# Performance work log

Measured on AMD Instinct MI355X. Metric: run time of the kernel, lower is better.

## Reference

```python
import jax, jax.numpy as jnp
import numpy as np

D = 512      # model_dim
H = 8        # num_heads
HD = D // H  # head_dim = 64
S = 196      # tokens per channel (14x14 grid)
CHANNELS = np.array([2, 4, 6, 4], dtype=np.int32)  # multiplex channels per sample


def setup_inputs() -> dict:
    key = jax.random.key(0)
    ks = jax.random.split(key, 8)
    C = int(CHANNELS.sum())  # 16
    n = lambda k, shp, s=1.0: jax.random.normal(k, shp, dtype=jnp.float32) * s
    return {
        "x_query": n(ks[0], (C, S, D)),
        "x_keyval": n(ks[1], (C, S, D)),
        "pos": n(ks[2], (C, S, D)),
        "channels": CHANNELS,
        "Wq": n(ks[3], (D, D), 0.02), "bq": jnp.zeros((D,), jnp.float32),
        "Wk": n(ks[4], (D, D), 0.02), "bk": jnp.zeros((D,), jnp.float32),
        "Wv": n(ks[5], (D, D), 0.02), "bv": jnp.zeros((D,), jnp.float32),
        "Wo": n(ks[6], (D, D), 0.02), "bo": jnp.zeros((D,), jnp.float32),
    }


def reference(x_query, x_keyval, pos, channels, Wq, bq, Wk, bk, Wv, bv, Wo, bo):
    C, S_, D_ = x_query.shape
    ch = np.asarray(channels)
    # segment id per packed token; segment i has length channels[i]*S (== cu_seq_len blocks)
    seg = np.repeat(np.arange(ch.shape[0]), ch * S_)                # [T] static
    block_mask = seg[:, None] == seg[None, :]                        # [T,T] static bool

    xq = x_query.reshape(-1, D_)   # [T,D]
    xk = x_keyval.reshape(-1, D_)
    p = pos.reshape(-1, D_)

    # positional embedding fused into Q/K before projection (query_pos/key_pos)
    q = ((xq + p) @ Wq + bq).reshape(-1, H, HD)
    k = ((xk + p) @ Wk + bk).reshape(-1, H, HD)
    v = (xk @ Wv + bv).reshape(-1, H, HD)

    scale = 1.0 / np.sqrt(HD)
    scores = jnp.einsum('qhd,khd->hqk', q, k) * scale               # [H,T,T]
    scores = jnp.where(block_mask[None], scores, jnp.float32(-1e30))
    attn = jax.nn.softmax(scores, axis=-1)
    out = jnp.einsum('hqk,khd->qhd', attn, v).reshape(-1, D_)       # [T,D]
    out = out @ Wo + bo
    return out.reshape(C, S_, D_)
```

## Files before the change

### kernel.cpp

```cpp
#include <hip/hip_runtime.h>
#include <hip/hip_bf16.h>


typedef short short8 __attribute__((ext_vector_type(8)));
typedef float f32x4 __attribute__((ext_vector_type(4)));

__device__ __forceinline__ float b2f(unsigned short u) {
    union { float f; unsigned int i; } x; x.i = ((unsigned int)u) << 16; return x.f;
}
__device__ __forceinline__ unsigned short f2b(float f) {
    union { float f; unsigned int i; } x; x.f = f;
    unsigned int r = x.i + 0x7fffu + ((x.i >> 16) & 1u);
    return (unsigned short)(r >> 16);
}

#define NE 1605632
#define WE 262144
#define GS 72

__launch_bounds__(256)
__global__ void prep(const float* __restrict__ xq, const float* __restrict__ xk,
                     const float* __restrict__ pos,
                     const float* __restrict__ W0, const float* __restrict__ W1,
                     const float* __restrict__ W2, const float* __restrict__ W3,
                     unsigned short* __restrict__ WF,
                     unsigned short* __restrict__ aqb, unsigned short* __restrict__ akb,
                     unsigned short* __restrict__ xkbb) {
    const int tid = threadIdx.x;
    if (blockIdx.z < 4) {
        if (blockIdx.x >= 128) return;
        const float* W = blockIdx.z == 0 ? W0 : blockIdx.z == 1 ? W1 : blockIdx.z == 2 ? W2 : W3;
        unsigned short* T = WF + (size_t)blockIdx.z * WE;
        const int s = blockIdx.x * 4 + (tid >> 6);
        const int f = s >> 4, t = s & 15;
        const int lane = tid & 63, quad = lane >> 4, l16 = lane & 15;
        short8 o;
        #pragma unroll
        for (int j = 0; j < 8; ++j)
            o[j] = (short)f2b(W[(size_t)(t * 32 + quad * 8 + j) * 512 + f * 16 + l16]);
        *(short8*)(T + (size_t)s * 512 + lane * 8) = o;
    } else {
        const size_t e = ((size_t)blockIdx.x * 256 + tid) * 8;
        f32x4 q0 = *(const f32x4*)(xq + e),  q1 = *(const f32x4*)(xq + e + 4);
        f32x4 k0 = *(const f32x4*)(xk + e),  k1 = *(const f32x4*)(xk + e + 4);
        f32x4 p0 = *(const f32x4*)(pos + e), p1 = *(const f32x4*)(pos + e + 4);
        short8 a, b, c;
        #pragma unroll
        for (int j = 0; j < 4; ++j) {
            a[j] = (short)f2b(q0[j] + p0[j]); a[4 + j] = (short)f2b(q1[j] + p1[j]);
            b[j] = (short)f2b(k0[j] + p0[j]); b[4 + j] = (short)f2b(k1[j] + p1[j]);
            c[j] = (short)f2b(k0[j]);         c[4 + j] = (short)f2b(k1[j]);
        }
        *(short8*)(aqb + e)  = a;
        *(short8*)(akb + e)  = b;
        *(short8*)(xkbb + e) = c;
    }
}

template <bool OUT_F32>
__device__ __forceinline__ void gemm_wave(const unsigned short* __restrict__ A,
                                          const unsigned short* __restrict__ WFw,
                                          const float* __restrict__ bias,
                                          void* __restrict__ C,
                                          int m0, int n0) {
    const int lane = threadIdx.x & 63;
    const int quad = lane >> 4, l16 = lane & 15;
    const int f0 = n0 >> 4;
    const unsigned short* Arow = A + (size_t)(m0 + l16) * 512 + quad * 8;
    const unsigned short* Bbase = WFw + (size_t)lane * 8;

    f32x4 acc[4] = {};
    #pragma unroll 4
    for (int t = 0; t < 16; ++t) {
        short8 af = *(const short8*)(Arow + t * 32);
        #pragma unroll
        for (int nt = 0; nt < 4; ++nt) {
            short8 bf = *(const short8*)(Bbase + (size_t)((f0 + nt) * 16 + t) * 512);
            acc[nt] = __builtin_amdgcn_mfma_f32_16x16x32_bf16(af, bf, acc[nt], 0, 0, 0);
        }
    }
    #pragma unroll
    for (int nt = 0; nt < 4; ++nt) {
        const int col = n0 + nt * 16 + l16;
        const float bv = bias[col];
        #pragma unroll
        for (int r = 0; r < 4; ++r) {
            const int row = m0 + quad * 4 + r;
            float cv = acc[nt][r] + bv;
            if constexpr (OUT_F32) ((float*)C)[(size_t)row * 512 + col] = cv;
            else ((unsigned short*)C)[(size_t)row * 512 + col] = f2b(cv);
        }
    }
}

__launch_bounds__(256)
__global__ void qkv_gemm(const unsigned short* __restrict__ aqb,
                         const unsigned short* __restrict__ akb,
                         const unsigned short* __restrict__ xkbb,
                         const unsigned short* __restrict__ WF,
                         const float* __restrict__ bq, const float* __restrict__ bk,
                         const float* __restrict__ bv,
                         unsigned short* __restrict__ qb, unsigned short* __restrict__ kb,
                         unsigned short* __restrict__ vb) {
    const unsigned short* A; const unsigned short* WFw; const float* bias; unsigned short* C;
    switch (blockIdx.z) {
        case 0:  A = aqb;  WFw = WF;          bias = bq; C = qb; break;
        case 1:  A = akb;  WFw = WF + WE;     bias = bk; C = kb; break;
        default: A = xkbb; WFw = WF + 2 * WE; bias = bv; C = vb; break;
    }
    gemm_wave<false>(A, WFw, bias, C, blockIdx.x * 64 + (threadIdx.x >> 6) * 16,
                     blockIdx.y * 64);
}

__launch_bounds__(256)
__global__ void out_gemm(const unsigned short* __restrict__ A,
                         const unsigned short* __restrict__ WFo,
                         const float* __restrict__ bo, float* __restrict__ out) {
    gemm_wave<true>(A, WFo, bo, out, blockIdx.x * 64 + (threadIdx.x >> 6) * 16,
                    blockIdx.y * 64);
}

__launch_bounds__(256)
__global__ void attn_seg(const unsigned short* __restrict__ q,
                         const unsigned short* __restrict__ k,
                         const unsigned short* __restrict__ v,
                         unsigned short* __restrict__ o) {
    __shared__ __align__(16) unsigned short Vt[64 * GS];
    __shared__ __align__(16) unsigned char  Pw[4][16 * 144];

    const int id = blockIdx.x;
    int h, off, L, qt;
    if (id < 152)      { h = id & 7; qt = id >> 3; off = 1176; L = 1176; }
    else if (id < 360) { int m = id - 152; h = m & 7; int s = m >> 3;
                         if (s < 13) { off = 392;  L = 784; qt = s; }
                         else        { off = 2352; L = 784; qt = s - 13; } }
    else               { int m = id - 360; h = m & 7; qt = m >> 3; off = 0; L = 392; }

    const int tid = threadIdx.x;
    const int wave = tid >> 6, lane = tid & 63;
    const int quad = lane >> 4, l16 = lane & 15;
    const int hb = h * 64;
    const int lastr = off + L - 1;

    int qrow = off + qt * 64 + wave * 16 + l16;
    if (qrow > lastr) qrow = lastr;
    const short8 qf0 = *(const short8*)(q + (size_t)qrow * 512 + hb + quad * 8);
    const short8 qf1 = *(const short8*)(q + (size_t)qrow * 512 + hb + 32 + quad * 8);

    const int skey = lane, sd = wave * 16;
    const int ntiles = (L + 63) >> 6;

    float lsum = 0.f;
    f32x4 oacc[4] = {};

    const unsigned short* kp = k + (size_t)off * 512 + hb + quad * 8;

    short8 kf[8];
    short8 vr0, vr1;
    {
        #pragma unroll
        for (int g = 0; g < 4; ++g) {
            const unsigned short* kr = kp + (size_t)(g * 16 + l16) * 512;
            kf[g * 2]     = *(const short8*)(kr);
            kf[g * 2 + 1] = *(const short8*)(kr + 32);
        }
        int krow = off + skey;
        vr0 = *(const short8*)(v + (size_t)krow * 512 + hb + sd);
        vr1 = *(const short8*)(v + (size_t)krow * 512 + hb + sd + 8);
    }
    unsigned char* Pme = Pw[wave];
    unsigned char* pwr = Pme + l16 * 144 + quad * 8;
    const unsigned char* prd = Pme + l16 * 144 + quad * 16;

    for (int b = 0; b < ntiles; ++b) {
        __syncthreads();
        #pragma unroll
        for (int j = 0; j < 8; ++j) {
            Vt[(sd + j) * GS + skey]     = (unsigned short)vr0[j];
            Vt[(sd + 8 + j) * GS + skey] = (unsigned short)vr1[j];
        }
        __syncthreads();
        if (b + 1 < ntiles) {
            int kk = (b + 1) * 64 + skey;
            int krow = off + (kk < L ? kk : L - 1);
            vr0 = *(const short8*)(v + (size_t)krow * 512 + hb + sd);
            vr1 = *(const short8*)(v + (size_t)krow * 512 + hb + sd + 8);
        }
        f32x4 sT[4];
        #pragma unroll
        for (int g = 0; g < 4; ++g) {
            f32x4 z = {0.f, 0.f, 0.f, 0.f};
            z     = __builtin_amdgcn_mfma_f32_16x16x32_bf16(kf[g * 2],     qf0, z, 0, 0, 0);
            sT[g] = __builtin_amdgcn_mfma_f32_16x16x32_bf16(kf[g * 2 + 1], qf1, z, 0, 0, 0);
        }
        if (b + 1 < ntiles) {
            const int nb = (b + 1) * 64;
            #pragma unroll
            for (int g = 0; g < 4; ++g) {
                int kk = nb + g * 16 + l16;
                const unsigned short* kr = kp + (size_t)(kk < L ? kk : L - 1) * 512;
                kf[g * 2]     = *(const short8*)(kr);
                kf[g * 2 + 1] = *(const short8*)(kr + 32);
            }
        }
        const int kbase = b * 64 + quad * 4;
        #pragma unroll
        for (int g = 0; g < 4; ++g) {
            float p[4];
            #pragma unroll
            for (int r = 0; r < 4; ++r) {
                const bool valid = (kbase + g * 16 + r) < L;
                p[r] = valid ? __expf(fminf(sT[g][r] * 0.125f, 30.f)) : 0.f;
                lsum += p[r];
            }
            #pragma unroll
            for (int i = 0; i < 2; ++i) {
                __hip_bfloat162 t = __float22bfloat162_rn(make_float2(p[2 * i], p[2 * i + 1]));
                *(unsigned int*)(pwr + g * 32 + i * 4) = *(unsigned int*)&t;
            }
        }
        short8 pa0 = *(const short8*)(prd);
        short8 pa1 = *(const short8*)(prd + 64);
        #pragma unroll
        for (int nt = 0; nt < 4; ++nt) {
            short8 vf0 = *(const short8*)(Vt + (nt * 16 + l16) * GS + quad * 8);
            short8 vf1 = *(const short8*)(Vt + (nt * 16 + l16) * GS + 32 + quad * 8);
            oacc[nt] = __builtin_amdgcn_mfma_f32_16x16x32_bf16(pa0, vf0, oacc[nt], 0, 0, 0);
            oacc[nt] = __builtin_amdgcn_mfma_f32_16x16x32_bf16(pa1, vf1, oacc[nt], 0, 0, 0);
        }
    }
    lsum += __shfl_xor(lsum, 16);
    lsum += __shfl_xor(lsum, 32);
    #pragma unroll
    for (int r = 0; r < 4; ++r) {
        const float srow = __shfl(lsum, (lane & 48) + quad * 4 + r);
        const float linv = 1.0f / srow;
        const int qi = qt * 64 + wave * 16 + quad * 4 + r;
        if (qi < L) {
            #pragma unroll
            for (int nt = 0; nt < 4; ++nt)
                o[(size_t)(off + qi) * 512 + hb + nt * 16 + l16] = f2b(oacc[nt][r] * linv);
        }
    }
}

extern "C" void kernel_launch(void* const* d_in, const int* in_sizes, int n_in,
                              void* d_out, int out_size, void* d_ws, size_t ws_size,
                              hipStream_t stream) {
    const float* xq  = (const float*)d_in[0];
    const float* xk  = (const float*)d_in[1];
    const float* pos = (const float*)d_in[2];
    const float* Wq = (const float*)d_in[4];
    const float* bq = (const float*)d_in[5];
    const float* Wk = (const float*)d_in[6];
    const float* bk = (const float*)d_in[7];
    const float* Wv = (const float*)d_in[8];
    const float* bv = (const float*)d_in[9];
    const float* Wo = (const float*)d_in[10];
    const float* bo = (const float*)d_in[11];
    float* out = (float*)d_out;

    unsigned short* ws = (unsigned short*)d_ws;
    unsigned short* qb   = ws;
    unsigned short* kb   = ws + NE;
    unsigned short* vb   = ws + (size_t)2 * NE;
    unsigned short* aqb  = ws + (size_t)3 * NE;
    unsigned short* akb  = ws + (size_t)4 * NE;
    unsigned short* xkbb = ws + (size_t)5 * NE;
    unsigned short* WF   = ws + (size_t)6 * NE;

    prep<<<dim3(784, 1, 5), 256, 0, stream>>>(xq, xk, pos, Wq, Wk, Wv, Wo,
                                              WF, aqb, akb, xkbb);
    qkv_gemm<<<dim3(49, 8, 3), 256, 0, stream>>>(aqb, akb, xkbb, WF, bq, bk, bv,
                                                 qb, kb, vb);
    attn_seg<<<dim3(416), 256, 0, stream>>>(qb, kb, vb, qb);
    out_gemm<<<dim3(49, 8), 256, 0, stream>>>(qb, WF + (size_t)3 * WE, bo, out);
}
```

Before: 159.8 us.

## Split key tiles across two wave groups per block and stage K in LDS

The attention block grows to 512 threads, forming two groups of four waves. Each group processes half of the key tiles for the same 64 query rows. Partial outputs and row sums are then merged through LDS before normalization; because the softmax uses a clamped exp with no running max, this merge is a plain sum. K tiles are now loaded cooperatively into shared memory instead of each wave loading its own copy from global memory, which cuts redundant global traffic. The aim is more parallelism per query tile and shorter serial key loops. In exchange it uses more LDS, adds an extra merge sync, and wastes one tile when the tile count is odd.

```diff
diff --git a/kernel.cpp b/kernel.cpp
--- a/kernel.cpp
+++ b/kernel.cpp
@@ -120,13 +120,12 @@
                     blockIdx.y * 64);
 }
 
-__launch_bounds__(256)
+__launch_bounds__(512)
 __global__ void attn_seg(const unsigned short* __restrict__ q,
                          const unsigned short* __restrict__ k,
                          const unsigned short* __restrict__ v,
                          unsigned short* __restrict__ o) {
-    __shared__ __align__(16) unsigned short Vt[64 * GS];
-    __shared__ __align__(16) unsigned char  Pw[4][16 * 144];
+    __shared__ __align__(16) unsigned char Lds[55296];
 
     const int id = blockIdx.x;
     int h, off, L, qt;
@@ -138,72 +137,68 @@
 
     const int tid = threadIdx.x;
     const int wave = tid >> 6, lane = tid & 63;
+    const int grp = wave >> 2, w4 = wave & 3;
     const int quad = lane >> 4, l16 = lane & 15;
     const int hb = h * 64;
     const int lastr = off + L - 1;
 
-    int qrow = off + qt * 64 + wave * 16 + l16;
+    unsigned short* Ks = (unsigned short*)(Lds + grp * 18432);
+    unsigned short* Vt = (unsigned short*)(Lds + grp * 18432 + 9216);
+    unsigned char*  Pme = Lds + 36864 + wave * 2304;
+
+    int qrow = off + qt * 64 + w4 * 16 + l16;
     if (qrow > lastr) qrow = lastr;
     const short8 qf0 = *(const short8*)(q + (size_t)qrow * 512 + hb + quad * 8);
     const short8 qf1 = *(const short8*)(q + (size_t)qrow * 512 + hb + 32 + quad * 8);
 
-    const int skey = lane, sd = wave * 16;
+    const int skey = lane, sd = w4 * 16;
     const int ntiles = (L + 63) >> 6;
+    const int nt0 = (ntiles + 1) >> 1;
 
     float lsum = 0.f;
     f32x4 oacc[4] = {};
 
-    const unsigned short* kp = k + (size_t)off * 512 + hb + quad * 8;
-
-    short8 kf[8];
-    short8 vr0, vr1;
+    short8 kr0, kr1, vr0, vr1;
     {
-        #pragma unroll
-        for (int g = 0; g < 4; ++g) {
-            const unsigned short* kr = kp + (size_t)(g * 16 + l16) * 512;
-            kf[g * 2]     = *(const short8*)(kr);
-            kf[g * 2 + 1] = *(const short8*)(kr + 32);
-        }
-        int krow = off + skey;
+        int kk = (grp ? nt0 : 0) * 64 + skey;
+        int krow = off + (kk < L ? kk : L - 1);
+        kr0 = *(const short8*)(k + (size_t)krow * 512 + hb + sd);
+        kr1 = *(const short8*)(k + (size_t)krow * 512 + hb + sd + 8);
         vr0 = *(const short8*)(v + (size_t)krow * 512 + hb + sd);
         vr1 = *(const short8*)(v + (size_t)krow * 512 + hb + sd + 8);
     }
-    unsigned char* Pme = Pw[wave];
     unsigned char* pwr = Pme + l16 * 144 + quad * 8;
     const unsigned char* prd = Pme + l16 * 144 + quad * 16;
 
-    for (int b = 0; b < ntiles; ++b) {
+    for (int i = 0; i < nt0; ++i) {
+        const int tg = (grp ? nt0 : 0) + i;
         __syncthreads();
+        *(short8*)(Ks + skey * GS + sd)     = kr0;
+        *(short8*)(Ks + skey * GS + sd + 8) = kr1;
         #pragma unroll
         for (int j = 0; j < 8; ++j) {
             Vt[(sd + j) * GS + skey]     = (unsigned short)vr0[j];
             Vt[(sd + 8 + j) * GS + skey] = (unsigned short)vr1[j];
         }
         __syncthreads();
-        if (b + 1 < ntiles) {
-            int kk = (b + 1) * 64 + skey;
+        if (i + 1 < nt0) {
+            int kk = (tg + 1) * 64 + skey;
             int krow = off + (kk < L ? kk : L - 1);
+            kr0 = *(const short8*)(k + (size_t)krow * 512 + hb + sd);
+            kr1 = *(const short8*)(k + (size_t)krow * 512 + hb + sd + 8);
             vr0 = *(const short8*)(v + (size_t)krow * 512 + hb + sd);
             vr1 = *(const short8*)(v + (size_t)krow * 512 + hb + sd + 8);
         }
         f32x4 sT[4];
         #pragma unroll
         for (int g = 0; g < 4; ++g) {
+            short8 kb0 = *(const short8*)(Ks + (g * 16 + l16) * GS + quad * 8);
+            short8 kb1 = *(const short8*)(Ks + (g * 16 + l16) * GS + 32 + quad * 8);
             f32x4 z = {0.f, 0.f, 0.f, 0.f};
-            z     = __builtin_amdgcn_mfma_f32_16x16x32_bf16(kf[g * 2],     qf0, z, 0, 0, 0);
-            sT[g] = __builtin_amdgcn_mfma_f32_16x16x32_bf16(kf[g * 2 + 1], qf1, z, 0, 0, 0);
-        }
-        if (b + 1 < ntiles) {
-            const int nb = (b + 1) * 64;
-            #pragma unroll
-            for (int g = 0; g < 4; ++g) {
-                int kk = nb + g * 16 + l16;
-                const unsigned short* kr = kp + (size_t)(kk < L ? kk : L - 1) * 512;
-                kf[g * 2]     = *(const short8*)(kr);
-                kf[g * 2 + 1] = *(const short8*)(kr + 32);
-            }
-        }
-        const int kbase = b * 64 + quad * 4;
+            z     = __builtin_amdgcn_mfma_f32_16x16x32_bf16(kb0, qf0, z, 0, 0, 0);
+            sT[g] = __builtin_amdgcn_mfma_f32_16x16x32_bf16(kb1, qf1, z, 0, 0, 0);
+        }
+        const int kbase = tg * 64 + quad * 4;
         #pragma unroll
         for (int g = 0; g < 4; ++g) {
             float p[4];
@@ -214,9 +209,9 @@
                 lsum += p[r];
             }
             #pragma unroll
-            for (int i = 0; i < 2; ++i) {
-                __hip_bfloat162 t = __float22bfloat162_rn(make_float2(p[2 * i], p[2 * i + 1]));
-                *(unsigned int*)(pwr + g * 32 + i * 4) = *(unsigned int*)&t;
+            for (int i2 = 0; i2 < 2; ++i2) {
+                __hip_bfloat162 t = __float22bfloat162_rn(make_float2(p[2 * i2], p[2 * i2 + 1]));
+                *(unsigned int*)(pwr + g * 32 + i2 * 4) = *(unsigned int*)&t;
             }
         }
         short8 pa0 = *(const short8*)(prd);
@@ -231,15 +226,33 @@
     }
     lsum += __shfl_xor(lsum, 16);
     lsum += __shfl_xor(lsum, 32);
-    #pragma unroll
-    for (int r = 0; r < 4; ++r) {
-        const float srow = __shfl(lsum, (lane & 48) + quad * 4 + r);
-        const float linv = 1.0f / srow;
-        const int qi = qt * 64 + wave * 16 + quad * 4 + r;
-        if (qi < L) {
-            #pragma unroll
-            for (int nt = 0; nt < 4; ++nt)
-                o[(size_t)(off + qi) * 512 + hb + nt * 16 + l16] = f2b(oacc[nt][r] * linv);
+
+    __syncthreads();
+    float* Mrg = (float*)(Lds + w4 * 5120 + lane * 80);
+    float* Ls  = (float*)(Lds + 20480);
+    if (grp == 1) {
+        #pragma unroll
+        for (int nt = 0; nt < 4; ++nt) *(f32x4*)(Mrg + nt * 4) = oacc[nt];
+        Ls[w4 * 64 + lane] = lsum;
+    }
+    __syncthreads();
+    if (grp == 0) {
+        lsum += Ls[w4 * 64 + lane];
+        #pragma unroll
+        for (int nt = 0; nt < 4; ++nt) {
+            f32x4 po = *(const f32x4*)(Mrg + nt * 4);
+            oacc[nt] += po;
+        }
+        #pragma unroll
+        for (int r = 0; r < 4; ++r) {
+            const float srow = __shfl(lsum, (lane & 48) + quad * 4 + r);
+            const float linv = 1.0f / srow;
+            const int qi = qt * 64 + w4 * 16 + quad * 4 + r;
+            if (qi < L) {
+                #pragma unroll
+                for (int nt = 0; nt < 4; ++nt)
+                    o[(size_t)(off + qi) * 512 + hb + nt * 16 + l16] = f2b(oacc[nt][r] * linv);
+            }
         }
     }
 }
@@ -273,6 +286,6 @@
                                               WF, aqb, akb, xkbb);
     qkv_gemm<<<dim3(49, 8, 3), 256, 0, stream>>>(aqb, akb, xkbb, WF, bq, bk, bv,
                                                  qb, kb, vb);
-    attn_seg<<<dim3(416), 256, 0, stream>>>(qb, kb, vb, qb);
+    attn_seg<<<dim3(416), 512, 0, stream>>>(qb, kb, vb, qb);
     out_gemm<<<dim3(49, 8), 256, 0, stream>>>(qb, WF + (size_t)3 * WE, bo, out);
 }
```

New measurement: 146.3 us. 1.09x faster.
